# Kernel optimization log

Hardware: AMD Instinct MI355X
Metric: run time of the kernel (lower is better)

## Reference

```python
import jax, jax.numpy as jnp
import numpy as np

N_USER, N_ITEM, N_HID = 100000, 150000, 64
N_LAYERS, S_LAYERS = 2, 2
N_NODES = N_USER + N_ITEM
E_UI, E_S = 1_000_000, 1_000_000
EPS = 1e-12
SLOPE = 0.5  # LeakyReLU(0.5)


def _spmm(rows, cols, vals, x, n):
    # sparse COO (rows, cols, vals) @ dense x -> [n, d]
    return jax.ops.segment_sum(vals[:, None] * x[cols], rows, num_segments=n)


def _leaky(x):
    return jnp.where(x >= 0, x, SLOPE * x)


def _l2norm(x):
    # F.normalize(p=2, dim=1), eps=1e-12
    n = jnp.linalg.norm(x, axis=1, keepdims=True)
    return x / jnp.maximum(n, EPS)


def setup_inputs() -> dict:
    key = jax.random.key(0)
    ks = jax.random.split(key, 10)
    return {
        "user_emb": jax.random.normal(ks[0], (N_USER, N_HID), jnp.float32) * 0.02,
        "item_emb": jax.random.normal(ks[1], (N_ITEM, N_HID), jnp.float32) * 0.02,
        "ui_weights": jax.random.normal(ks[2], (N_LAYERS, N_HID, N_HID), jnp.float32) * 0.125,
        "social_weights": jax.random.normal(ks[3], (S_LAYERS, N_HID, N_HID), jnp.float32) * 0.125,
        "ui_rows": jax.random.randint(ks[4], (E_UI,), 0, N_NODES, jnp.int32),
        "ui_cols": jax.random.randint(ks[5], (E_UI,), 0, N_NODES, jnp.int32),
        "ui_vals": jax.random.uniform(ks[6], (E_UI,), jnp.float32),
        "social_rows": jax.random.randint(ks[7], (E_S,), 0, N_USER, jnp.int32),
        "social_cols": jax.random.randint(ks[8], (E_S,), 0, N_USER, jnp.int32),
        "social_vals": jax.random.uniform(ks[9], (E_S,), jnp.float32),
    }


def reference(user_emb, item_emb, ui_weights, social_weights,
              ui_rows, ui_cols, ui_vals,
              social_rows, social_cols, social_vals):
    # user-item GCN branch
    u, i = user_emb, item_emb
    ui_embs = [jnp.concatenate([u, i], axis=0)]
    for l in range(N_LAYERS):
        node = jnp.concatenate([u, i], axis=0) @ ui_weights[l]      # [N_NODES, H]
        node = _leaky(_spmm(ui_rows, ui_cols, ui_vals, node, N_NODES))
        u, i = node[:N_USER], node[N_USER:]
        ui_embs.append(_l2norm(node))
    ui_emb = ui_embs[0] + ui_embs[1] + ui_embs[2]

    # social GCN branch
    s = user_emb
    s_embs = [s]
    for l in range(S_LAYERS):
        s = _leaky(_spmm(social_rows, social_cols, social_vals, s @ social_weights[l], N_USER))
        s_embs.append(_l2norm(s))
    social_emb = s_embs[0] + s_embs[1] + s_embs[2]
    return ui_emb, social_emb
```

## Files before the change

### kernel.cpp

```cpp
#include <hip/hip_runtime.h>

#define N_USER   100000
#define N_ITEM   150000
#define N_NODES  250000
#define N_HID    64
#define E_UI     1000000
#define E_S      1000000
#define N_TOT    (N_NODES + N_USER)
#define E_TOT    (E_UI + E_S)

#define BR     64
#define CH     4096
#define NBBIN  ((E_TOT + CH - 1) / CH)
#define RPB    1024
#define RPB_SH 10
#define NBKT   ((N_TOT + RPB - 1) / RPB)
#define NBKTP  512
#define LSTR   344
#define ASTR   72
#define BCAP_PAD 16384
#define BCAP_STD 12288

typedef unsigned long long ull;
typedef __attribute__((ext_vector_type(8))) short short8v;
typedef __attribute__((ext_vector_type(4))) float f32x4;

__device__ __forceinline__ unsigned short f_to_bf(float f) {
    unsigned u = __float_as_uint(f);
    u += 0x7FFF + ((u >> 16) & 1);
    return (unsigned short)(u >> 16);
}
__device__ __forceinline__ float bf_to_f(unsigned short s) {
    return __uint_as_float((unsigned)s << 16);
}
__device__ __forceinline__ unsigned pack_bf2(float a, float b) {
    return (unsigned)f_to_bf(a) | ((unsigned)f_to_bf(b) << 16);
}

__global__ __launch_bounds__(256) void embcast(const float* __restrict__ u,
                                               const float* __restrict__ it,
                                               unsigned short* __restrict__ embBf) {
    int i = blockIdx.x * 256 + threadIdx.x;
    const int n8 = N_NODES * N_HID / 8;
    if (i >= n8) return;
    size_t base = (size_t)i * 8;
    const size_t nu = (size_t)N_USER * N_HID;
    const float* src = (base < nu) ? u + base : it + (base - nu);
    float4 a = *(const float4*)src;
    float4 b = *(const float4*)(src + 4);
    uint4 o;
    o.x = pack_bf2(a.x, a.y); o.y = pack_bf2(a.z, a.w);
    o.z = pack_bf2(b.x, b.y); o.w = pack_bf2(b.z, b.w);
    *(uint4*)&embBf[base] = o;
}

__global__ __launch_bounds__(512) void bin_local(const int* __restrict__ ui_rows,
                                                 const int* __restrict__ ui_cols,
                                                 const float* __restrict__ ui_vals,
                                                 const int* __restrict__ s_rows,
                                                 const int* __restrict__ s_cols,
                                                 const float* __restrict__ s_vals,
                                                 ull* __restrict__ pairsA,
                                                 int* __restrict__ lstartAll) {
    __shared__ int hist[NBKTP];
    __shared__ int lstart[NBKTP];
    __shared__ int cnt2[NBKTP];
    const int t = threadIdx.x;
    hist[t] = 0; cnt2[t] = 0;
    __syncthreads();

    const int e0 = blockIdx.x * CH;
    const int n  = min(CH, E_TOT - e0);

    for (int i = t; i < n; i += 512) {
        int g = e0 + i, r;
        if (g < E_UI) r = ui_rows[g];
        else          r = N_NODES + s_rows[g - E_UI];
        atomicAdd(&hist[r >> RPB_SH], 1);
    }
    __syncthreads();

    int v = hist[t];
    lstart[t] = v;
    __syncthreads();
    for (int off = 1; off < NBKTP; off <<= 1) {
        int a = (t >= off) ? lstart[t - off] : 0;
        __syncthreads();
        lstart[t] += a;
        __syncthreads();
    }
    int ex = lstart[t] - v;
    __syncthreads();
    lstart[t] = ex;
    if (t <= NBKT) lstartAll[blockIdx.x * LSTR + t] = ex;
    __syncthreads();

    for (int i = t; i < n; i += 512) {
        int g = e0 + i, r, c; float val;
        if (g < E_UI) { r = ui_rows[g];            c = ui_cols[g];            val = ui_vals[g]; }
        else          { int k = g - E_UI;
                        r = N_NODES + s_rows[k];   c = N_NODES + s_cols[k];   val = s_vals[k]; }
        int b = r >> RPB_SH;
        ull entry = ((ull)__float_as_uint(val) << 32) |
                    ((ull)(unsigned)(r & (RPB - 1)) << 19) | (unsigned)c;
        int l = atomicAdd(&cnt2[b], 1);
        pairsA[(size_t)blockIdx.x * CH + lstart[b] + l] = entry;
    }
}

template <bool PAD>
__global__ __launch_bounds__(512) void fine_gather2(const ull* __restrict__ pairsA,
                                                    const int* __restrict__ lstartAll,
                                                    int* __restrict__ rowStart,
                                                    int* __restrict__ bucketEnd,
                                                    ull* __restrict__ pairs,
                                                    int bcap) {
    __shared__ int cur[RPB];
    __shared__ int sc[RPB];
    const int b = blockIdx.x, t = threadIdx.x;
    const int r0 = b * RPB;
    const int nr = min(RPB, N_TOT - r0);
    const int base = b * bcap;

    cur[t] = 0; cur[t + 512] = 0;
    __syncthreads();

    const int q    = t >> 4;
    const int lane = t & 15;

    for (int blk = q; blk < NBBIN; blk += 32) {
        int s = lstartAll[blk * LSTR + b];
        int e = lstartAll[blk * LSTR + b + 1];
        const ull* src = pairsA + (size_t)blk * CH;
        for (int j = s + lane; j < e; j += 16)
            atomicAdd(&cur[(int)((src[j] >> 19) & (RPB - 1))], 1);
    }
    __syncthreads();

    int c0 = cur[t], c1 = cur[t + 512];
    int p0 = PAD ? ((c0 + 7) & ~7) : c0;
    int p1 = PAD ? ((c1 + 7) & ~7) : c1;
    sc[t] = p0; sc[t + 512] = p1;
    __syncthreads();
    for (int off = 1; off < RPB; off <<= 1) {
        int a = (t >= off) ? sc[t - off] : 0;
        int bb = (t + 512 >= off) ? sc[t + 512 - off] : 0;
        __syncthreads();
        sc[t] += a; sc[t + 512] += bb;
        __syncthreads();
    }
    int inc0 = sc[t], inc1 = sc[t + 512];
    __syncthreads();
    int st0 = base + inc0 - p0;
    int st1 = base + inc1 - p1;
    cur[t] = st0;            cur[t + 512] = st1;
    sc[t]  = st0 + p0;       sc[t + 512]  = st1 + p1;
    if (t < nr)        rowStart[r0 + t] = st0;
    if (t + 512 < nr)  rowStart[r0 + t + 512] = st1;
    if (t == 511) {
        bucketEnd[b] = st1 + p1;
        if (b == NBKT - 1) rowStart[N_TOT] = st1 + p1;
    }
    __syncthreads();

    for (int blk = q; blk < NBBIN; blk += 32) {
        int s = lstartAll[blk * LSTR + b];
        int e = lstartAll[blk * LSTR + b + 1];
        const ull* src = pairsA + (size_t)blk * CH;
        for (int j = s + lane; j < e; j += 16) {
            ull en = src[j];
            int rLow = (int)((en >> 19) & (RPB - 1));
            int pos = atomicAdd(&cur[rLow], 1);
            pairs[pos] = (en & 0xFFFFFFFF00000000ull) | (en & 0x7FFFFull);
        }
    }
    if (PAD) {
        __syncthreads();
        for (int i = t; i < nr; i += 512) {
            int end = sc[i];
            for (int j = cur[i]; j < end; ++j) pairs[j] = 0;
        }
    }
}

template <int LAYER, bool PADDED>
__global__ __launch_bounds__(256) void spmm_m(const ull* __restrict__ pairs,
                                              const int* __restrict__ rowStart,
                                              const int* __restrict__ bucketEnd,
                                              const unsigned short* __restrict__ embBf,
                                              const unsigned short* __restrict__ B2in,
                                              unsigned short* __restrict__ B2out,
                                              const unsigned short* __restrict__ tmp12in,
                                              unsigned short* __restrict__ tmp12out,
                                              const float* __restrict__ Wui,
                                              const float* __restrict__ Wsoc,
                                              float* __restrict__ out_ui,
                                              float* __restrict__ out_s,
                                              int uiBlocks) {
    __shared__ unsigned short Wb[N_HID][ASTR];
    __shared__ unsigned short agg[4][16][ASTR];
    const int tid = threadIdx.x;
    const bool isUI = (int)blockIdx.x < uiBlocks;
    const int bl    = isUI ? blockIdx.x : blockIdx.x - uiBlocks;
    const int rbeg  = isUI ? bl * BR : N_NODES + bl * BR;
    const int rlim  = isUI ? min(BR, N_NODES - bl * BR) : min(BR, N_USER - bl * BR);

    const float* W = isUI ? Wui : Wsoc;
    for (int idx = tid; idx < N_HID * N_HID; idx += 256) {
        int r = idx >> 6, c = idx & 63;
        Wb[c][r] = f_to_bf(W[idx]);
    }
    __syncthreads();

    const int w = tid >> 6;
    if (w * 16 >= rlim) return;
    const int s = tid & 15;
    const int g = (tid >> 4) & 3;

    short8v bfrag[4][2];
#pragma unroll
    for (int nt = 0; nt < 4; ++nt)
#pragma unroll
        for (int kt = 0; kt < 2; ++kt)
            bfrag[nt][kt] = *(const short8v*)&Wb[nt * 16 + s][kt * 32 + g * 8];

    const unsigned short* gsrc = (LAYER == 1) ? embBf : B2in;

    int sB[4], eB[4];
#pragma unroll
    for (int i = 0; i < 4; ++i) {
        int r = rbeg + w * 16 + i * 4 + g;
        sB[i] = rowStart[r];
        int e = rowStart[r + 1];
        if (((r + 1) & (RPB - 1)) == 0)
            e = bucketEnd[r >> RPB_SH];
        eB[i] = e;
    }

    for (int i = 0; i < 4; ++i) {
        float4 acc = make_float4(0.f, 0.f, 0.f, 0.f);
        if (PADDED) {
            for (int j = sB[i]; j < eB[i]; j += 8) {
                ull p[8];
#pragma unroll
                for (int k = 0; k < 8; ++k) p[k] = pairs[j + k];
                ushort4 raw[8];
#pragma unroll
                for (int k = 0; k < 8; ++k) {
                    unsigned c = (unsigned)p[k] & 0x7FFFFu;
                    if (LAYER == 1 && c >= N_NODES) c -= N_NODES;
                    raw[k] = *(const ushort4*)(gsrc + (size_t)c * N_HID + s * 4);
                }
#pragma unroll
                for (int k = 0; k < 8; ++k) {
                    float v = __uint_as_float((unsigned)(p[k] >> 32));
                    acc.x = fmaf(v, bf_to_f(raw[k].x), acc.x);
                    acc.y = fmaf(v, bf_to_f(raw[k].y), acc.y);
                    acc.z = fmaf(v, bf_to_f(raw[k].z), acc.z);
                    acc.w = fmaf(v, bf_to_f(raw[k].w), acc.w);
                }
            }
        } else {
            int e0 = eB[i];
            for (int j = sB[i]; j < e0; j += 8) {
                int last = e0 - 1;
                ull p[8];
#pragma unroll
                for (int k = 0; k < 8; ++k) p[k] = pairs[min(j + k, last)];
                ushort4 raw[8];
#pragma unroll
                for (int k = 0; k < 8; ++k) {
                    unsigned c = (unsigned)p[k] & 0x7FFFFu;
                    if (LAYER == 1 && c >= N_NODES) c -= N_NODES;
                    raw[k] = *(const ushort4*)(gsrc + (size_t)c * N_HID + s * 4);
                }
#pragma unroll
                for (int k = 0; k < 8; ++k) {
                    float v = (j + k < e0) ? __uint_as_float((unsigned)(p[k] >> 32)) : 0.f;
                    acc.x = fmaf(v, bf_to_f(raw[k].x), acc.x);
                    acc.y = fmaf(v, bf_to_f(raw[k].y), acc.y);
                    acc.z = fmaf(v, bf_to_f(raw[k].z), acc.z);
                    acc.w = fmaf(v, bf_to_f(raw[k].w), acc.w);
                }
            }
        }
        uint2 pk;
        pk.x = pack_bf2(acc.x, acc.y);
        pk.y = pack_bf2(acc.z, acc.w);
        *(uint2*)&agg[w][i * 4 + g][s * 4] = pk;
    }
    asm volatile("s_waitcnt lgkmcnt(0)" ::: "memory");
    __builtin_amdgcn_sched_barrier(0);

    short8v a0 = *(const short8v*)&agg[w][s][g * 8];
    short8v a1 = *(const short8v*)&agg[w][s][32 + g * 8];
    f32x4 c[4];
    const f32x4 zero4 = {0.f, 0.f, 0.f, 0.f};
#pragma unroll
    for (int nt = 0; nt < 4; ++nt) {
        c[nt] = __builtin_amdgcn_mfma_f32_16x16x32_bf16(a0, bfrag[nt][0], zero4, 0, 0, 0);
        c[nt] = __builtin_amdgcn_mfma_f32_16x16x32_bf16(a1, bfrag[nt][1], c[nt], 0, 0, 0);
    }

    float lv[4][4];
    float ss[4] = {0.f, 0.f, 0.f, 0.f};
#pragma unroll
    for (int nt = 0; nt < 4; ++nt)
#pragma unroll
        for (int r = 0; r < 4; ++r) {
            float z = c[nt][r];
            float l = (z >= 0.f) ? z : 0.5f * z;
            lv[nt][r] = l;
            ss[r] = fmaf(l, l, ss[r]);
        }
#pragma unroll
    for (int r = 0; r < 4; ++r) {
        float t = ss[r];
        t += __shfl_xor(t, 1, 64);
        t += __shfl_xor(t, 2, 64);
        t += __shfl_xor(t, 4, 64);
        t += __shfl_xor(t, 8, 64);
        ss[r] = 1.f / fmaxf(sqrtf(t), 1e-12f);
    }

#pragma unroll
    for (int r = 0; r < 4; ++r) {
        int R = rbeg + w * 16 + g * 4 + r;
        if (LAYER == 1) {
            size_t eRow = isUI ? (size_t)R : (size_t)(R - N_NODES);
#pragma unroll
            for (int nt = 0; nt < 4; ++nt) {
                int col = nt * 16 + s;
                float eb = bf_to_f(embBf[eRow * N_HID + col]);
                tmp12out[(size_t)R * N_HID + col] = f_to_bf(fmaf(lv[nt][r], ss[r], eb));
                B2out[(size_t)R * N_HID + col]    = f_to_bf(lv[nt][r]);
            }
        } else {
            float* op = isUI ? out_ui + (size_t)R * N_HID
                             : out_s  + (size_t)(R - N_NODES) * N_HID;
#pragma unroll
            for (int nt = 0; nt < 4; ++nt) {
                int col = nt * 16 + s;
                float tb = bf_to_f(tmp12in[(size_t)R * N_HID + col]);
                op[col] = fmaf(lv[nt][r], ss[r], tb);
            }
        }
    }
}

__global__ __launch_bounds__(256) void init_concat(const float* __restrict__ u,
                                                   const float* __restrict__ it,
                                                   float* __restrict__ A,
                                                   float* __restrict__ out) {
    int i = blockIdx.x * 256 + threadIdx.x;
    const int nu4 = N_USER * N_HID / 4;
    const int nt4 = N_NODES * N_HID / 4;
    if (i >= nt4) return;
    float4 v = (i < nu4) ? ((const float4*)u)[i] : ((const float4*)it)[i - nu4];
    ((float4*)A)[i]   = v;
    ((float4*)out)[i] = v;
}

__global__ __launch_bounds__(256) void copy2(const float* __restrict__ src,
                                             float* __restrict__ d0,
                                             float* __restrict__ d1, int n4) {
    int i = blockIdx.x * 256 + threadIdx.x;
    if (i >= n4) return;
    float4 v = ((const float4*)src)[i];
    ((float4*)d0)[i] = v;
    ((float4*)d1)[i] = v;
}

__global__ __launch_bounds__(256) void gemm64(const float* __restrict__ X,
                                              const float* __restrict__ W,
                                              float* __restrict__ Y, int nrows) {
    __shared__ float Ws[N_HID * N_HID];
    int tid = threadIdx.x;
#pragma unroll
    for (int c = 0; c < 16; ++c) Ws[c * 256 + tid] = W[c * 256 + tid];
    __syncthreads();
    int row = blockIdx.x * 256 + tid;
    if (row >= nrows) return;
    float x[N_HID];
    const float4* xr = (const float4*)(X + (size_t)row * N_HID);
#pragma unroll
    for (int c = 0; c < 16; ++c) {
        float4 v = xr[c];
        x[4*c+0] = v.x; x[4*c+1] = v.y; x[4*c+2] = v.z; x[4*c+3] = v.w;
    }
    float4* y4 = (float4*)(Y + (size_t)row * N_HID);
    for (int jc = 0; jc < 16; ++jc) {
        float4 a = make_float4(0.f,0.f,0.f,0.f);
#pragma unroll
        for (int k = 0; k < N_HID; ++k) {
            float4 wv = *((const float4*)&Ws[k * N_HID + jc * 4]);
            a.x += x[k]*wv.x; a.y += x[k]*wv.y; a.z += x[k]*wv.z; a.w += x[k]*wv.w;
        }
        y4[jc] = a;
    }
}

__global__ __launch_bounds__(256) void spmm_scatter(const int* __restrict__ rows,
                                                    const int* __restrict__ cols,
                                                    const float* __restrict__ vals,
                                                    const float* __restrict__ X,
                                                    float* __restrict__ Y, int nedges) {
    long long t = (long long)blockIdx.x * 256 + threadIdx.x;
    int e = (int)(t >> 6);
    int h = (int)(t & 63);
    if (e >= nedges) return;
    atomicAdd(&Y[rows[e] * N_HID + h], vals[e] * X[cols[e] * N_HID + h]);
}

__global__ __launch_bounds__(256) void leaky_norm_acc(float* __restrict__ Y,
                                                      float* __restrict__ out, int nrows) {
    int row = blockIdx.x * 4 + (threadIdx.x >> 6);
    int h   = threadIdx.x & 63;
    if (row >= nrows) return;
    int idx = row * N_HID + h;
    float v = Y[idx];
    v = (v >= 0.f) ? v : 0.5f * v;
    Y[idx] = v;
    float s = v * v;
#pragma unroll
    for (int off = 32; off > 0; off >>= 1) s += __shfl_xor(s, off, 64);
    out[idx] += v / fmaxf(sqrtf(s), 1e-12f);
}

extern "C" void kernel_launch(void* const* d_in, const int* in_sizes, int n_in,
                              void* d_out, int out_size, void* d_ws, size_t ws_size,
                              hipStream_t stream) {
    const float* user_emb = (const float*)d_in[0];
    const float* item_emb = (const float*)d_in[1];
    const float* ui_w     = (const float*)d_in[2];
    const float* s_w      = (const float*)d_in[3];
    const int*   ui_rows  = (const int*)d_in[4];
    const int*   ui_cols  = (const int*)d_in[5];
    const float* ui_vals  = (const float*)d_in[6];
    const int*   s_rows   = (const int*)d_in[7];
    const int*   s_cols   = (const int*)d_in[8];
    const float* s_vals   = (const float*)d_in[9];

    float* out_ui = (float*)d_out;
    float* out_s  = (float*)d_out + (size_t)N_NODES * N_HID;

    const size_t szUI  = (size_t)N_NODES * N_HID * sizeof(float);
    const size_t szEB  = (size_t)N_NODES * N_HID * sizeof(short);
    const size_t szBF  = (size_t)N_TOT   * N_HID * sizeof(short);
    const size_t rsPad = 1400832;
    const size_t lsSz  = 1 << 20;

    const int uiBlocks = (N_NODES + BR - 1) / BR;
    const int sBlocks  = (N_USER  + BR - 1) / BR;
    const int nbEC     = (N_NODES * N_HID / 8 + 255) / 256;

    const size_t pairsCapPad = (size_t)NBKT * BCAP_PAD * 8;
    const size_t pairsCapStd = (size_t)NBKT * BCAP_STD * 8;

    const size_t needPad = szEB + 2 * szBF + pairsCapPad + rsPad + lsSz;
    const size_t needStd = szEB + 2 * szBF + pairsCapStd + rsPad + lsSz;

    if (ws_size >= needStd) {
        const bool padded = (ws_size >= needPad);
        const int  bcap   = padded ? BCAP_PAD : BCAP_STD;
        const size_t pairsCap = padded ? pairsCapPad : pairsCapStd;

        unsigned short* embBf = (unsigned short*)d_ws;
        unsigned short* B2    = (unsigned short*)((char*)d_ws + szEB);
        unsigned short* tmp12 = (unsigned short*)((char*)d_ws + szEB + szBF);
        char* p = (char*)d_ws + szEB + 2 * szBF;
        ull* pairs     = (ull*)p;            p += pairsCap;
        int* rowStart  = (int*)p;            p += rsPad;
        int* lstartAll = (int*)p;
        int* bucketEnd = lstartAll + (size_t)NBBIN * LSTR;
        ull* pairsA    = (ull*)tmp12;

        embcast<<<nbEC, 256, 0, stream>>>(user_emb, item_emb, embBf);
        bin_local<<<NBBIN, 512, 0, stream>>>(ui_rows, ui_cols, ui_vals,
                                             s_rows, s_cols, s_vals,
                                             pairsA, lstartAll);
        if (padded)
            fine_gather2<true><<<NBKT, 512, 0, stream>>>(pairsA, lstartAll,
                                                         rowStart, bucketEnd,
                                                         pairs, bcap);
        else
            fine_gather2<false><<<NBKT, 512, 0, stream>>>(pairsA, lstartAll,
                                                          rowStart, bucketEnd,
                                                          pairs, bcap);

        const int grid = uiBlocks + sBlocks;
        const float* Wui2 = ui_w + N_HID * N_HID;
        const float* Ws2  = s_w  + N_HID * N_HID;
        if (padded) {
            spmm_m<1, true><<<grid, 256, 0, stream>>>(pairs, rowStart, bucketEnd, embBf,
                                                      nullptr, B2, nullptr, tmp12,
                                                      ui_w, s_w, out_ui, out_s, uiBlocks);
            spmm_m<2, true><<<grid, 256, 0, stream>>>(pairs, rowStart, bucketEnd, embBf,
                                                      B2, nullptr, tmp12, nullptr,
                                                      Wui2, Ws2, out_ui, out_s, uiBlocks);
        } else {
            spmm_m<1, false><<<grid, 256, 0, stream>>>(pairs, rowStart, bucketEnd, embBf,
                                                       nullptr, B2, nullptr, tmp12,
                                                       ui_w, s_w, out_ui, out_s, uiBlocks);
            spmm_m<2, false><<<grid, 256, 0, stream>>>(pairs, rowStart, bucketEnd, embBf,
                                                       B2, nullptr, tmp12, nullptr,
                                                       Wui2, Ws2, out_ui, out_s, uiBlocks);
        }
        return;
    }

    float* A = (float*)d_ws;
    float* B = (float*)((char*)d_ws + szUI);
    init_concat<<<(N_NODES * N_HID / 4 + 255) / 256, 256, 0, stream>>>(
        user_emb, item_emb, A, out_ui);
    for (int l = 0; l < 2; ++l) {
        gemm64<<<(N_NODES + 255) / 256, 256, 0, stream>>>(
            A, ui_w + l * N_HID * N_HID, B, N_NODES);
        hipMemsetAsync(A, 0, szUI, stream);
        spmm_scatter<<<(int)(((long long)E_UI * 64) / 256), 256, 0, stream>>>(
            ui_rows, ui_cols, ui_vals, B, A, E_UI);
        leaky_norm_acc<<<(N_NODES + 3) / 4, 256, 0, stream>>>(A, out_ui, N_NODES);
    }
    copy2<<<(N_USER * N_HID / 4 + 255) / 256, 256, 0, stream>>>(
        user_emb, A, out_s, N_USER * N_HID / 4);
    const size_t sBytes = (size_t)N_USER * N_HID * sizeof(float);
    for (int l = 0; l < 2; ++l) {
        gemm64<<<(N_USER + 255) / 256, 256, 0, stream>>>(
            A, s_w + l * N_HID * N_HID, B, N_USER);
        hipMemsetAsync(A, 0, sBytes, stream);
        spmm_scatter<<<(int)(((long long)E_S * 64) / 256), 256, 0, stream>>>(
            s_rows, s_cols, s_vals, B, A, E_S);
        leaky_norm_acc<<<(N_USER + 3) / 4, 256, 0, stream>>>(A, out_s, N_USER);
    }
}
```

Before: 234.8 us.

## Fuse embedding cast into binning kernel, duplicate user rows, prefetch next row's pairs

The bf16 embedding cast is folded into the edge-binning kernel as extra blocks, so one launch goes away. The bf16 table is extended with a copy of the user rows placed after the nodes. Social-branch column indices then address it directly, which drops the mask and subtract in the gather and the row remap in the layer-1 epilogue. The padded SpMM path now preloads the first 8 pairs of the next row while the current row is processed, to hide pair-load latency. The cost is a larger cast, more workspace, and the assumption that the low 32 bits of each pair hold only the column index.

```diff
diff --git a/kernel.cpp b/kernel.cpp
--- a/kernel.cpp
+++ b/kernel.cpp
@@ -37,35 +37,41 @@
     return (unsigned)f_to_bf(a) | ((unsigned)f_to_bf(b) << 16);
 }
 
-__global__ __launch_bounds__(256) void embcast(const float* __restrict__ u,
-                                               const float* __restrict__ it,
-                                               unsigned short* __restrict__ embBf) {
-    int i = blockIdx.x * 256 + threadIdx.x;
-    const int n8 = N_NODES * N_HID / 8;
-    if (i >= n8) return;
-    size_t base = (size_t)i * 8;
-    const size_t nu = (size_t)N_USER * N_HID;
-    const float* src = (base < nu) ? u + base : it + (base - nu);
-    float4 a = *(const float4*)src;
-    float4 b = *(const float4*)(src + 4);
-    uint4 o;
-    o.x = pack_bf2(a.x, a.y); o.y = pack_bf2(a.z, a.w);
-    o.z = pack_bf2(b.x, b.y); o.w = pack_bf2(b.z, b.w);
-    *(uint4*)&embBf[base] = o;
-}
-
-__global__ __launch_bounds__(512) void bin_local(const int* __restrict__ ui_rows,
-                                                 const int* __restrict__ ui_cols,
-                                                 const float* __restrict__ ui_vals,
-                                                 const int* __restrict__ s_rows,
-                                                 const int* __restrict__ s_cols,
-                                                 const float* __restrict__ s_vals,
-                                                 ull* __restrict__ pairsA,
-                                                 int* __restrict__ lstartAll) {
+__global__ __launch_bounds__(512) void bin_embcast(const int* __restrict__ ui_rows,
+                                                   const int* __restrict__ ui_cols,
+                                                   const float* __restrict__ ui_vals,
+                                                   const int* __restrict__ s_rows,
+                                                   const int* __restrict__ s_cols,
+                                                   const float* __restrict__ s_vals,
+                                                   ull* __restrict__ pairsA,
+                                                   int* __restrict__ lstartAll,
+                                                   const float* __restrict__ u,
+                                                   const float* __restrict__ it,
+                                                   unsigned short* __restrict__ embBf) {
     __shared__ int hist[NBKTP];
     __shared__ int lstart[NBKTP];
     __shared__ int cnt2[NBKTP];
     const int t = threadIdx.x;
+
+    if ((int)blockIdx.x >= NBBIN) {
+        int i = ((int)blockIdx.x - NBBIN) * 512 + t;
+        const int n8 = N_TOT * N_HID / 8;
+        if (i >= n8) return;
+        size_t base = (size_t)i * 8;
+        const size_t nu = (size_t)N_USER * N_HID;
+        const size_t nn = (size_t)N_NODES * N_HID;
+        const float* src = (base < nu) ? u + base
+                         : (base < nn) ? it + (base - nu)
+                                       : u + (base - nn);
+        float4 a = *(const float4*)src;
+        float4 b = *(const float4*)(src + 4);
+        uint4 o;
+        o.x = pack_bf2(a.x, a.y); o.y = pack_bf2(a.z, a.w);
+        o.z = pack_bf2(b.x, b.y); o.w = pack_bf2(b.z, b.w);
+        *(uint4*)&embBf[base] = o;
+        return;
+    }
+
     hist[t] = 0; cnt2[t] = 0;
     __syncthreads();
 
@@ -237,30 +243,51 @@
         eB[i] = e;
     }
 
-    for (int i = 0; i < 4; ++i) {
-        float4 acc = make_float4(0.f, 0.f, 0.f, 0.f);
-        if (PADDED) {
-            for (int j = sB[i]; j < eB[i]; j += 8) {
-                ull p[8];
-#pragma unroll
-                for (int k = 0; k < 8; ++k) p[k] = pairs[j + k];
-                ushort4 raw[8];
-#pragma unroll
-                for (int k = 0; k < 8; ++k) {
-                    unsigned c = (unsigned)p[k] & 0x7FFFFu;
-                    if (LAYER == 1 && c >= N_NODES) c -= N_NODES;
-                    raw[k] = *(const ushort4*)(gsrc + (size_t)c * N_HID + s * 4);
-                }
-#pragma unroll
-                for (int k = 0; k < 8; ++k) {
-                    float v = __uint_as_float((unsigned)(p[k] >> 32));
-                    acc.x = fmaf(v, bf_to_f(raw[k].x), acc.x);
-                    acc.y = fmaf(v, bf_to_f(raw[k].y), acc.y);
-                    acc.z = fmaf(v, bf_to_f(raw[k].z), acc.z);
-                    acc.w = fmaf(v, bf_to_f(raw[k].w), acc.w);
+    if (PADDED) {
+        ull p[8];
+#pragma unroll
+        for (int k = 0; k < 8; ++k) p[k] = pairs[sB[0] + k];
+
+        for (int i = 0; i < 4; ++i) {
+            ull pc[8];
+#pragma unroll
+            for (int k = 0; k < 8; ++k) pc[k] = p[k];
+            if (i < 3) {
+                int nb = sB[i + 1];
+#pragma unroll
+                for (int k = 0; k < 8; ++k) p[k] = pairs[nb + k];
+            }
+            float4 acc = make_float4(0.f, 0.f, 0.f, 0.f);
+            int j = sB[i], e0 = eB[i];
+            if (j < e0) {
+                while (true) {
+                    ushort4 raw[8];
+#pragma unroll
+                    for (int k = 0; k < 8; ++k)
+                        raw[k] = *(const ushort4*)(gsrc +
+                                   (size_t)(unsigned)pc[k] * N_HID + s * 4);
+#pragma unroll
+                    for (int k = 0; k < 8; ++k) {
+                        float v = __uint_as_float((unsigned)(pc[k] >> 32));
+                        acc.x = fmaf(v, bf_to_f(raw[k].x), acc.x);
+                        acc.y = fmaf(v, bf_to_f(raw[k].y), acc.y);
+                        acc.z = fmaf(v, bf_to_f(raw[k].z), acc.z);
+                        acc.w = fmaf(v, bf_to_f(raw[k].w), acc.w);
+                    }
+                    j += 8;
+                    if (j >= e0) break;
+#pragma unroll
+                    for (int k = 0; k < 8; ++k) pc[k] = pairs[j + k];
                 }
             }
-        } else {
+            uint2 pk;
+            pk.x = pack_bf2(acc.x, acc.y);
+            pk.y = pack_bf2(acc.z, acc.w);
+            *(uint2*)&agg[w][i * 4 + g][s * 4] = pk;
+        }
+    } else {
+        for (int i = 0; i < 4; ++i) {
+            float4 acc = make_float4(0.f, 0.f, 0.f, 0.f);
             int e0 = eB[i];
             for (int j = sB[i]; j < e0; j += 8) {
                 int last = e0 - 1;
@@ -269,11 +296,9 @@
                 for (int k = 0; k < 8; ++k) p[k] = pairs[min(j + k, last)];
                 ushort4 raw[8];
 #pragma unroll
-                for (int k = 0; k < 8; ++k) {
-                    unsigned c = (unsigned)p[k] & 0x7FFFFu;
-                    if (LAYER == 1 && c >= N_NODES) c -= N_NODES;
-                    raw[k] = *(const ushort4*)(gsrc + (size_t)c * N_HID + s * 4);
-                }
+                for (int k = 0; k < 8; ++k)
+                    raw[k] = *(const ushort4*)(gsrc +
+                               (size_t)(unsigned)p[k] * N_HID + s * 4);
 #pragma unroll
                 for (int k = 0; k < 8; ++k) {
                     float v = (j + k < e0) ? __uint_as_float((unsigned)(p[k] >> 32)) : 0.f;
@@ -283,11 +308,11 @@
                     acc.w = fmaf(v, bf_to_f(raw[k].w), acc.w);
                 }
             }
-        }
-        uint2 pk;
-        pk.x = pack_bf2(acc.x, acc.y);
-        pk.y = pack_bf2(acc.z, acc.w);
-        *(uint2*)&agg[w][i * 4 + g][s * 4] = pk;
+            uint2 pk;
+            pk.x = pack_bf2(acc.x, acc.y);
+            pk.y = pack_bf2(acc.z, acc.w);
+            *(uint2*)&agg[w][i * 4 + g][s * 4] = pk;
+        }
     }
     asm volatile("s_waitcnt lgkmcnt(0)" ::: "memory");
     __builtin_amdgcn_sched_barrier(0);
@@ -327,11 +352,10 @@
     for (int r = 0; r < 4; ++r) {
         int R = rbeg + w * 16 + g * 4 + r;
         if (LAYER == 1) {
-            size_t eRow = isUI ? (size_t)R : (size_t)(R - N_NODES);
 #pragma unroll
             for (int nt = 0; nt < 4; ++nt) {
                 int col = nt * 16 + s;
-                float eb = bf_to_f(embBf[eRow * N_HID + col]);
+                float eb = bf_to_f(embBf[(size_t)R * N_HID + col]);
                 tmp12out[(size_t)R * N_HID + col] = f_to_bf(fmaf(lv[nt][r], ss[r], eb));
                 B2out[(size_t)R * N_HID + col]    = f_to_bf(lv[nt][r]);
             }
@@ -445,20 +469,19 @@
     float* out_s  = (float*)d_out + (size_t)N_NODES * N_HID;
 
     const size_t szUI  = (size_t)N_NODES * N_HID * sizeof(float);
-    const size_t szEB  = (size_t)N_NODES * N_HID * sizeof(short);
     const size_t szBF  = (size_t)N_TOT   * N_HID * sizeof(short);
     const size_t rsPad = 1400832;
     const size_t lsSz  = 1 << 20;
 
     const int uiBlocks = (N_NODES + BR - 1) / BR;
     const int sBlocks  = (N_USER  + BR - 1) / BR;
-    const int nbEC     = (N_NODES * N_HID / 8 + 255) / 256;
+    const int nbEC     = (N_TOT * N_HID / 8 + 511) / 512;
 
     const size_t pairsCapPad = (size_t)NBKT * BCAP_PAD * 8;
     const size_t pairsCapStd = (size_t)NBKT * BCAP_STD * 8;
 
-    const size_t needPad = szEB + 2 * szBF + pairsCapPad + rsPad + lsSz;
-    const size_t needStd = szEB + 2 * szBF + pairsCapStd + rsPad + lsSz;
+    const size_t needPad = 3 * szBF + pairsCapPad + rsPad + lsSz;
+    const size_t needStd = 3 * szBF + pairsCapStd + rsPad + lsSz;
 
     if (ws_size >= needStd) {
         const bool padded = (ws_size >= needPad);
@@ -466,19 +489,19 @@
         const size_t pairsCap = padded ? pairsCapPad : pairsCapStd;
 
         unsigned short* embBf = (unsigned short*)d_ws;
-        unsigned short* B2    = (unsigned short*)((char*)d_ws + szEB);
-        unsigned short* tmp12 = (unsigned short*)((char*)d_ws + szEB + szBF);
-        char* p = (char*)d_ws + szEB + 2 * szBF;
+        unsigned short* B2    = (unsigned short*)((char*)d_ws + szBF);
+        unsigned short* tmp12 = (unsigned short*)((char*)d_ws + 2 * szBF);
+        char* p = (char*)d_ws + 3 * szBF;
         ull* pairs     = (ull*)p;            p += pairsCap;
         int* rowStart  = (int*)p;            p += rsPad;
         int* lstartAll = (int*)p;
         int* bucketEnd = lstartAll + (size_t)NBBIN * LSTR;
         ull* pairsA    = (ull*)tmp12;
 
-        embcast<<<nbEC, 256, 0, stream>>>(user_emb, item_emb, embBf);
-        bin_local<<<NBBIN, 512, 0, stream>>>(ui_rows, ui_cols, ui_vals,
-                                             s_rows, s_cols, s_vals,
-                                             pairsA, lstartAll);
+        bin_embcast<<<NBBIN + nbEC, 512, 0, stream>>>(ui_rows, ui_cols, ui_vals,
+                                                      s_rows, s_cols, s_vals,
+                                                      pairsA, lstartAll,
+                                                      user_emb, item_emb, embBf);
         if (padded)
             fine_gather2<true><<<NBKT, 512, 0, stream>>>(pairsA, lstartAll,
                                                          rowStart, bucketEnd,
```

Result: slower. 249.1 us (+6.1%).
